# Performance work log

Hardware: AMD Instinct MI355X
Metric: run time of the kernel (lower is better)

Reference implementation:

```python
import jax, jax.numpy as jnp
import numpy as np


def setup_inputs() -> dict:
    key = jax.random.key(0)
    ks = jax.random.split(key, 6)
    B, C, H, W = 16, 192, 224, 224
    MAX_SEG = 196
    img = jax.random.normal(ks[0], (B, 3, H, W), dtype=jnp.float32)
    features = jax.random.normal(ks[1], (B, C, H, W), dtype=jnp.float32)
    segments = jax.random.randint(ks[2], (B, H, W), 0, MAX_SEG, dtype=jnp.int64)
    centroid_coords = jax.random.uniform(ks[3], (B, MAX_SEG, 2), dtype=jnp.float32) * jnp.array([W, H], dtype=jnp.float32)
    pos_W = jax.random.normal(ks[4], (2, C), dtype=jnp.float32) * 0.02
    pos_b = jax.random.normal(ks[5], (C,), dtype=jnp.float32) * 0.02
    return {"img": img, "features": features, "segments": segments,
            "centroid_coords": centroid_coords, "pos_W": pos_W, "pos_b": pos_b,
            "max_segments": MAX_SEG}


def reference(img, features, segments, centroid_coords, pos_W, pos_b, max_segments):
    B, C, Hf, Wf = features.shape
    H, W = img.shape[2], img.shape[3]
    # flatten pixels: [B*Hf*Wf, C]
    feats_flat = features.transpose(0, 2, 3, 1).reshape(-1, C)
    # per-batch-unique segment ids: b * max_segments + seg
    seg_flat = segments.reshape(B, Hf * Wf)
    uniq_ids = (jnp.arange(B, dtype=seg_flat.dtype)[:, None] * max_segments + seg_flat).reshape(-1)
    dim_size = B * max_segments
    # scatter_mean = segment_sum / clamp(count, 1)
    sums = jax.ops.segment_sum(feats_flat, uniq_ids, num_segments=dim_size)
    counts = jax.ops.segment_sum(jnp.ones((feats_flat.shape[0],), feats_flat.dtype),
                                 uniq_ids, num_segments=dim_size)
    embeddings = (sums / jnp.maximum(counts, 1.0)[:, None]).reshape(B, max_segments, C)
    # positional embedding of normalized centroids (x/W, y/H)
    scale = jnp.array([1.0 / W, 1.0 / H], dtype=centroid_coords.dtype)
    pos = (centroid_coords * scale) @ pos_W + pos_b  # [B, n_centroids, C]
    # pad/truncate pos to max_segments (here n_centroids == max_segments)
    n_centroids = pos.shape[1]
    if n_centroids > max_segments:
        pos_padded = pos[:, :max_segments, :]
    else:
        pos_padded = jnp.zeros((B, max_segments, C), pos.dtype).at[:, :n_centroids, :].set(pos)
    return embeddings + pos_padded
```

## Files before the change

### kernel.cpp

```cpp
#include <hip/hip_runtime.h>

#define BATCH 16
#define CHAN 192
#define HW 50176
#define NSEG 196
#define NSEGT 13
#define PIXSPLIT 8
#define PPB (HW / PIXSPLIT)
#define KSTEPS (PPB / 32)

typedef __attribute__((ext_vector_type(8))) short short8;
typedef __attribute__((ext_vector_type(4))) float f32x4;
typedef __attribute__((ext_vector_type(4))) int   i32x4;

__device__ __forceinline__ short bfc(float x) {
    unsigned u = __float_as_uint(x);
    return (short)((u + 0x8000u) >> 16);
}

__global__ __launch_bounds__(384, 3) void accum_mfma(
        const float* __restrict__ feat,
        const int*   __restrict__ seg,
        float*       __restrict__ out) {
    __shared__ short8 abuf[NSEGT * 64];

    const int tid  = threadIdx.x;
    const int wave = tid >> 6;
    const int lane = tid & 63;
    const int quad = lane >> 4;
    const int m    = lane & 15;

    const int b      = blockIdx.z;
    const int cbase  = (blockIdx.y * 6 + wave) * 16;
    const int pstart = blockIdx.x * PPB;

    const int*   sptr = seg  + (size_t)b * HW + pstart;
    const float* fptr = feat + ((size_t)b * CHAN + cbase + m) * HW + pstart;

    f32x4 acc[NSEGT];
#pragma unroll
    for (int t = 0; t < NSEGT; ++t) acc[t] = (f32x4)0.0f;

    i32x4 s0 = *(const i32x4*)(sptr + quad * 8);
    i32x4 s1 = *(const i32x4*)(sptr + quad * 8 + 4);
    f32x4 f0 = *(const f32x4*)(fptr + quad * 8);
    f32x4 f1 = *(const f32x4*)(fptr + quad * 8 + 4);

    for (int kk = 0; kk < KSTEPS; ++kk) {
        __syncthreads();
        const int sv[8] = {s0.x, s0.y, s0.z, s0.w, s1.x, s1.y, s1.z, s1.w};
        for (int t = wave; t < NSEGT; t += 6) {
            const int target = t * 16 + m;
            short8 af;
#pragma unroll
            for (int j = 0; j < 8; ++j)
                af[j] = (sv[j] == target) ? (short)0x3F80 : (short)0;
            abuf[t * 64 + lane] = af;
        }
        __syncthreads();

        short8 bf;
        bf[0] = bfc(f0.x); bf[1] = bfc(f0.y); bf[2] = bfc(f0.z); bf[3] = bfc(f0.w);
        bf[4] = bfc(f1.x); bf[5] = bfc(f1.y); bf[6] = bfc(f1.z); bf[7] = bfc(f1.w);

        const int pn = (kk + 1 < KSTEPS ? kk + 1 : kk) * 32;
        s0 = *(const i32x4*)(sptr + pn + quad * 8);
        s1 = *(const i32x4*)(sptr + pn + quad * 8 + 4);
        f0 = *(const f32x4*)(fptr + pn + quad * 8);
        f1 = *(const f32x4*)(fptr + pn + quad * 8 + 4);

#pragma unroll
        for (int t = 0; t < NSEGT; ++t) {
            short8 af = abuf[t * 64 + lane];
            acc[t] = __builtin_amdgcn_mfma_f32_16x16x32_bf16(af, bf, acc[t], 0, 0, 0);
        }
    }

    float* obase = out + ((size_t)b * NSEG) * CHAN + cbase + m;
#pragma unroll
    for (int t = 0; t < NSEGT; ++t) {
#pragma unroll
        for (int r = 0; r < 4; ++r) {
            const int s = t * 16 + quad * 4 + r;
            if (s < NSEG) atomicAdd(obase + (size_t)s * CHAN, acc[t][r]);
        }
    }
}

__global__ __launch_bounds__(256) void count_kernel(const int* __restrict__ seg,
                                                    int* __restrict__ counts) {
    __shared__ int cnt[NSEG];
    const int tid = threadIdx.x;
    if (tid < NSEG) cnt[tid] = 0;
    __syncthreads();
    const int b = blockIdx.y;
    const int4* sp = (const int4*)(seg + (size_t)b * HW + blockIdx.x * 1024);
    int4 s4 = sp[tid];
    atomicAdd(&cnt[s4.x], 1);
    atomicAdd(&cnt[s4.y], 1);
    atomicAdd(&cnt[s4.z], 1);
    atomicAdd(&cnt[s4.w], 1);
    __syncthreads();
    if (tid < NSEG) atomicAdd(&counts[b * NSEG + tid], cnt[tid]);
}

__global__ __launch_bounds__(256) void finalize_kernel(float* __restrict__ out,
                                                       const int* __restrict__ counts,
                                                       const float* __restrict__ coords,
                                                       const float* __restrict__ posW,
                                                       const float* __restrict__ posb) {
    const int idx = blockIdx.x * 256 + threadIdx.x;
    if (idx >= BATCH * NSEG * CHAN) return;
    const int c = idx % CHAN;
    const int s = (idx / CHAN) % NSEG;
    const int b = idx / (CHAN * NSEG);
    const float cntf = (float)max(counts[b * NSEG + s], 1);
    const float x = coords[(b * NSEG + s) * 2 + 0] * (1.0f / 224.0f);
    const float y = coords[(b * NSEG + s) * 2 + 1] * (1.0f / 224.0f);
    const float pos = x * posW[c] + y * posW[CHAN + c] + posb[c];
    out[idx] = out[idx] / cntf + pos;
}

extern "C" void kernel_launch(void* const* d_in, const int* in_sizes, int n_in,
                              void* d_out, int out_size, void* d_ws, size_t ws_size,
                              hipStream_t stream) {
    const float* feat   = (const float*)d_in[1];
    const int*   seg    = (const int*)d_in[2];
    const float* coords = (const float*)d_in[3];
    const float* posW   = (const float*)d_in[4];
    const float* posb   = (const float*)d_in[5];
    float* out    = (float*)d_out;
    int*   counts = (int*)d_ws;

    hipMemsetAsync(out, 0, (size_t)BATCH * NSEG * CHAN * sizeof(float), stream);
    hipMemsetAsync(counts, 0, (size_t)BATCH * NSEG * sizeof(int), stream);

    count_kernel<<<dim3(HW / 1024, BATCH), 256, 0, stream>>>(seg, counts);
    accum_mfma<<<dim3(PIXSPLIT, 2, BATCH), 384, 0, stream>>>(feat, seg, out);

    const int n = BATCH * NSEG * CHAN;
    finalize_kernel<<<dim3((n + 255) / 256), 256, 0, stream>>>(out, counts, coords, posW, posb);
}
```

Before: 948.5 us.

## Replace one-hot MFMA segment sum with LDS atomic scatter accumulation

Drops the bf16 one-hot-matrix MFMA formulation and instead scatters fp32 features into a padded per-block LDS table of segment sums with shared-memory atomics, then flushes the table to global memory with atomics. The per-segment count is folded into the same kernel, which removes the separate count kernel, and counts become floats. This avoids the 13x redundant one-hot MFMA work and the bf16 rounding. In exchange it relies on LDS atomic throughput under contention and uses about 77KB of LDS per 1024-thread block, which limits occupancy.

```diff
diff --git a/kernel.cpp b/kernel.cpp
--- a/kernel.cpp
+++ b/kernel.cpp
@@ -4,108 +4,75 @@
 #define CHAN 192
 #define HW 50176
 #define NSEG 196
-#define NSEGT 13
-#define PIXSPLIT 8
-#define PPB (HW / PIXSPLIT)
-#define KSTEPS (PPB / 32)
+#define CHALF 96
+#define PAD 97
+#define PIXCHUNK 3136
+#define NGROUP 49
+#define CPW 6
+#define CNT_ROW (NSEG * PAD)
+#define LDS_FLOATS (NSEG * PAD + NSEG)
 
-typedef __attribute__((ext_vector_type(8))) short short8;
-typedef __attribute__((ext_vector_type(4))) float f32x4;
-typedef __attribute__((ext_vector_type(4))) int   i32x4;
-
-__device__ __forceinline__ short bfc(float x) {
-    unsigned u = __float_as_uint(x);
-    return (short)((u + 0x8000u) >> 16);
-}
-
-__global__ __launch_bounds__(384, 3) void accum_mfma(
+__global__ __launch_bounds__(1024, 8) void accum_scatter(
         const float* __restrict__ feat,
         const int*   __restrict__ seg,
-        float*       __restrict__ out) {
-    __shared__ short8 abuf[NSEGT * 64];
+        float*       __restrict__ out,
+        float*       __restrict__ cnt) {
+    __shared__ float lds[LDS_FLOATS];
 
-    const int tid  = threadIdx.x;
-    const int wave = tid >> 6;
-    const int lane = tid & 63;
-    const int quad = lane >> 4;
-    const int m    = lane & 15;
+    const int tid   = threadIdx.x;
+    const int wave  = tid >> 6;
+    const int lane  = tid & 63;
+    const int b     = blockIdx.z;
+    const int cbase = blockIdx.y * CHALF;
+    const int pstart = blockIdx.x * PIXCHUNK;
+    const int lc0   = wave * CPW;
 
-    const int b      = blockIdx.z;
-    const int cbase  = (blockIdx.y * 6 + wave) * 16;
-    const int pstart = blockIdx.x * PPB;
+    for (int i = tid; i < LDS_FLOATS; i += 1024) lds[i] = 0.0f;
+    __syncthreads();
 
-    const int*   sptr = seg  + (size_t)b * HW + pstart;
-    const float* fptr = feat + ((size_t)b * CHAN + cbase + m) * HW + pstart;
+    const int*   sp  = seg  + (size_t)b * HW + pstart + lane;
+    const float* fp0 = feat + ((size_t)b * CHAN + cbase + lc0) * HW + pstart + lane;
+    const bool docount = (blockIdx.y == 0) && (wave == 0);
 
-    f32x4 acc[NSEGT];
+    int   s_cur = sp[0];
+    float v_cur[CPW];
 #pragma unroll
-    for (int t = 0; t < NSEGT; ++t) acc[t] = (f32x4)0.0f;
+    for (int j = 0; j < CPW; ++j) v_cur[j] = fp0[(size_t)j * HW];
 
-    i32x4 s0 = *(const i32x4*)(sptr + quad * 8);
-    i32x4 s1 = *(const i32x4*)(sptr + quad * 8 + 4);
-    f32x4 f0 = *(const f32x4*)(fptr + quad * 8);
-    f32x4 f1 = *(const f32x4*)(fptr + quad * 8 + 4);
+    for (int g = 0; g < NGROUP; ++g) {
+        int   s_nxt = 0;
+        float v_nxt[CPW];
+        if (g + 1 < NGROUP) {
+            const int poff = (g + 1) * 64;
+            s_nxt = sp[poff];
+            const float* fp = fp0 + poff;
+#pragma unroll
+            for (int j = 0; j < CPW; ++j) v_nxt[j] = fp[(size_t)j * HW];
+        }
 
-    for (int kk = 0; kk < KSTEPS; ++kk) {
-        __syncthreads();
-        const int sv[8] = {s0.x, s0.y, s0.z, s0.w, s1.x, s1.y, s1.z, s1.w};
-        for (int t = wave; t < NSEGT; t += 6) {
-            const int target = t * 16 + m;
-            short8 af;
+        if (docount) atomicAdd(lds + CNT_ROW + s_cur, 1.0f);
+        float* lrow = lds + s_cur * PAD + lc0;
 #pragma unroll
-            for (int j = 0; j < 8; ++j)
-                af[j] = (sv[j] == target) ? (short)0x3F80 : (short)0;
-            abuf[t * 64 + lane] = af;
-        }
-        __syncthreads();
+        for (int j = 0; j < CPW; ++j) atomicAdd(lrow + j, v_cur[j]);
 
-        short8 bf;
-        bf[0] = bfc(f0.x); bf[1] = bfc(f0.y); bf[2] = bfc(f0.z); bf[3] = bfc(f0.w);
-        bf[4] = bfc(f1.x); bf[5] = bfc(f1.y); bf[6] = bfc(f1.z); bf[7] = bfc(f1.w);
+        s_cur = s_nxt;
+#pragma unroll
+        for (int j = 0; j < CPW; ++j) v_cur[j] = v_nxt[j];
+    }
+    __syncthreads();
 
-        const int pn = (kk + 1 < KSTEPS ? kk + 1 : kk) * 32;
-        s0 = *(const i32x4*)(sptr + pn + quad * 8);
-        s1 = *(const i32x4*)(sptr + pn + quad * 8 + 4);
-        f0 = *(const f32x4*)(fptr + pn + quad * 8);
-        f1 = *(const f32x4*)(fptr + pn + quad * 8 + 4);
-
-#pragma unroll
-        for (int t = 0; t < NSEGT; ++t) {
-            short8 af = abuf[t * 64 + lane];
-            acc[t] = __builtin_amdgcn_mfma_f32_16x16x32_bf16(af, bf, acc[t], 0, 0, 0);
-        }
+    float* obase = out + ((size_t)b * NSEG) * CHAN + cbase;
+    for (int i = tid; i < NSEG * CHALF; i += 1024) {
+        const int s  = i / CHALF;
+        const int lc = i - s * CHALF;
+        atomicAdd(obase + (size_t)s * CHAN + lc, lds[s * PAD + lc]);
     }
-
-    float* obase = out + ((size_t)b * NSEG) * CHAN + cbase + m;
-#pragma unroll
-    for (int t = 0; t < NSEGT; ++t) {
-#pragma unroll
-        for (int r = 0; r < 4; ++r) {
-            const int s = t * 16 + quad * 4 + r;
-            if (s < NSEG) atomicAdd(obase + (size_t)s * CHAN, acc[t][r]);
-        }
-    }
-}
-
-__global__ __launch_bounds__(256) void count_kernel(const int* __restrict__ seg,
-                                                    int* __restrict__ counts) {
-    __shared__ int cnt[NSEG];
-    const int tid = threadIdx.x;
-    if (tid < NSEG) cnt[tid] = 0;
-    __syncthreads();
-    const int b = blockIdx.y;
-    const int4* sp = (const int4*)(seg + (size_t)b * HW + blockIdx.x * 1024);
-    int4 s4 = sp[tid];
-    atomicAdd(&cnt[s4.x], 1);
-    atomicAdd(&cnt[s4.y], 1);
-    atomicAdd(&cnt[s4.z], 1);
-    atomicAdd(&cnt[s4.w], 1);
-    __syncthreads();
-    if (tid < NSEG) atomicAdd(&counts[b * NSEG + tid], cnt[tid]);
+    if (blockIdx.y == 0 && tid < NSEG)
+        atomicAdd(cnt + b * NSEG + tid, lds[CNT_ROW + tid]);
 }
 
 __global__ __launch_bounds__(256) void finalize_kernel(float* __restrict__ out,
-                                                       const int* __restrict__ counts,
+                                                       const float* __restrict__ counts,
                                                        const float* __restrict__ coords,
                                                        const float* __restrict__ posW,
                                                        const float* __restrict__ posb) {
@@ -114,7 +81,7 @@
     const int c = idx % CHAN;
     const int s = (idx / CHAN) % NSEG;
     const int b = idx / (CHAN * NSEG);
-    const float cntf = (float)max(counts[b * NSEG + s], 1);
+    const float cntf = fmaxf(counts[b * NSEG + s], 1.0f);
     const float x = coords[(b * NSEG + s) * 2 + 0] * (1.0f / 224.0f);
     const float y = coords[(b * NSEG + s) * 2 + 1] * (1.0f / 224.0f);
     const float pos = x * posW[c] + y * posW[CHAN + c] + posb[c];
@@ -130,13 +97,12 @@
     const float* posW   = (const float*)d_in[4];
     const float* posb   = (const float*)d_in[5];
     float* out    = (float*)d_out;
-    int*   counts = (int*)d_ws;
+    float* counts = (float*)d_ws;
 
     hipMemsetAsync(out, 0, (size_t)BATCH * NSEG * CHAN * sizeof(float), stream);
-    hipMemsetAsync(counts, 0, (size_t)BATCH * NSEG * sizeof(int), stream);
+    hipMemsetAsync(counts, 0, (size_t)BATCH * NSEG * sizeof(float), stream);
 
-    count_kernel<<<dim3(HW / 1024, BATCH), 256, 0, stream>>>(seg, counts);
-    accum_mfma<<<dim3(PIXSPLIT, 2, BATCH), 384, 0, stream>>>(feat, seg, out);
+    accum_scatter<<<dim3(16, 2, BATCH), 1024, 0, stream>>>(feat, seg, out, counts);
 
     const int n = BATCH * NSEG * CHAN;
     finalize_kernel<<<dim3((n + 255) / 256), 256, 0, stream>>>(out, counts, coords, posW, posb);
```

Result: slower. 1.403 ms (+47.9%).

## Build one-hot operands in registers, fuse counting, and reduce partials instead of atomics

Applied to the files above, without the earlier changes.

Removes the shared-memory one-hot staging buffer and both block barriers per k-step, so each lane now builds its one-hot A fragments in registers. Segment counting moves into the accumulation kernel, done by one wave per block, which removes a separate launch. The pixel split doubles to give more blocks, and when the workspace is large enough each block writes its partial sums to a buffer that a fused reduce/finalize kernel adds up, replacing the global float atomics. The cost is redundant compare work in every wave, extra partial-buffer traffic, and a serialized count path in wave 0.

```diff
diff --git a/kernel.cpp b/kernel.cpp
--- a/kernel.cpp
+++ b/kernel.cpp
@@ -5,7 +5,7 @@
 #define HW 50176
 #define NSEG 196
 #define NSEGT 13
-#define PIXSPLIT 8
+#define PIXSPLIT 16
 #define PPB (HW / PIXSPLIT)
 #define KSTEPS (PPB / 32)
 
@@ -21,8 +21,10 @@
 __global__ __launch_bounds__(384, 3) void accum_mfma(
         const float* __restrict__ feat,
         const int*   __restrict__ seg,
-        float*       __restrict__ out) {
-    __shared__ short8 abuf[NSEGT * 64];
+        float*       __restrict__ dst,
+        int*         __restrict__ counts,
+        const int partial) {
+    __shared__ int scnt[NSEG];
 
     const int tid  = threadIdx.x;
     const int wave = tid >> 6;
@@ -33,6 +35,11 @@
     const int b      = blockIdx.z;
     const int cbase  = (blockIdx.y * 6 + wave) * 16;
     const int pstart = blockIdx.x * PPB;
+
+    const bool docount = (blockIdx.y == 0) && (wave == 0);
+    if (docount) {
+        for (int i = lane; i < NSEG; i += 64) scnt[i] = 0;
+    }
 
     const int*   sptr = seg  + (size_t)b * HW + pstart;
     const float* fptr = feat + ((size_t)b * CHAN + cbase + m) * HW + pstart;
@@ -47,61 +54,85 @@
     f32x4 f1 = *(const f32x4*)(fptr + quad * 8 + 4);
 
     for (int kk = 0; kk < KSTEPS; ++kk) {
-        __syncthreads();
         const int sv[8] = {s0.x, s0.y, s0.z, s0.w, s1.x, s1.y, s1.z, s1.w};
-        for (int t = wave; t < NSEGT; t += 6) {
-            const int target = t * 16 + m;
-            short8 af;
-#pragma unroll
-            for (int j = 0; j < 8; ++j)
-                af[j] = (sv[j] == target) ? (short)0x3F80 : (short)0;
-            abuf[t * 64 + lane] = af;
-        }
-        __syncthreads();
 
         short8 bf;
         bf[0] = bfc(f0.x); bf[1] = bfc(f0.y); bf[2] = bfc(f0.z); bf[3] = bfc(f0.w);
         bf[4] = bfc(f1.x); bf[5] = bfc(f1.y); bf[6] = bfc(f1.z); bf[7] = bfc(f1.w);
 
+        if (docount && m == 0) {
+#pragma unroll
+            for (int j = 0; j < 8; ++j) atomicAdd(&scnt[sv[j]], 1);
+        }
+
         const int pn = (kk + 1 < KSTEPS ? kk + 1 : kk) * 32;
-        s0 = *(const i32x4*)(sptr + pn + quad * 8);
-        s1 = *(const i32x4*)(sptr + pn + quad * 8 + 4);
-        f0 = *(const f32x4*)(fptr + pn + quad * 8);
-        f1 = *(const f32x4*)(fptr + pn + quad * 8 + 4);
+        i32x4 s0n = *(const i32x4*)(sptr + pn + quad * 8);
+        i32x4 s1n = *(const i32x4*)(sptr + pn + quad * 8 + 4);
+        f32x4 f0n = *(const f32x4*)(fptr + pn + quad * 8);
+        f32x4 f1n = *(const f32x4*)(fptr + pn + quad * 8 + 4);
+
+        int d[8];
+#pragma unroll
+        for (int j = 0; j < 8; ++j) d[j] = sv[j] - m;
 
 #pragma unroll
         for (int t = 0; t < NSEGT; ++t) {
-            short8 af = abuf[t * 64 + lane];
+            short8 af;
+#pragma unroll
+            for (int j = 0; j < 8; ++j)
+                af[j] = (d[j] == t * 16) ? (short)0x3F80 : (short)0;
             acc[t] = __builtin_amdgcn_mfma_f32_16x16x32_bf16(af, bf, acc[t], 0, 0, 0);
         }
+
+        s0 = s0n; s1 = s1n; f0 = f0n; f1 = f1n;
     }
 
-    float* obase = out + ((size_t)b * NSEG) * CHAN + cbase + m;
+    if (partial) {
+        float* obase = dst + (((size_t)blockIdx.x * BATCH + b) * NSEG) * CHAN + cbase + m;
 #pragma unroll
-    for (int t = 0; t < NSEGT; ++t) {
+        for (int t = 0; t < NSEGT; ++t) {
 #pragma unroll
-        for (int r = 0; r < 4; ++r) {
-            const int s = t * 16 + quad * 4 + r;
-            if (s < NSEG) atomicAdd(obase + (size_t)s * CHAN, acc[t][r]);
+            for (int r = 0; r < 4; ++r) {
+                const int s = t * 16 + quad * 4 + r;
+                if (s < NSEG) obase[(size_t)s * CHAN] = acc[t][r];
+            }
         }
+    } else {
+        float* obase = dst + ((size_t)b * NSEG) * CHAN + cbase + m;
+#pragma unroll
+        for (int t = 0; t < NSEGT; ++t) {
+#pragma unroll
+            for (int r = 0; r < 4; ++r) {
+                const int s = t * 16 + quad * 4 + r;
+                if (s < NSEG) atomicAdd(obase + (size_t)s * CHAN, acc[t][r]);
+            }
+        }
+    }
+    if (docount) {
+        for (int i = lane; i < NSEG; i += 64) atomicAdd(&counts[b * NSEG + i], scnt[i]);
     }
 }
 
-__global__ __launch_bounds__(256) void count_kernel(const int* __restrict__ seg,
-                                                    int* __restrict__ counts) {
-    __shared__ int cnt[NSEG];
-    const int tid = threadIdx.x;
-    if (tid < NSEG) cnt[tid] = 0;
-    __syncthreads();
-    const int b = blockIdx.y;
-    const int4* sp = (const int4*)(seg + (size_t)b * HW + blockIdx.x * 1024);
-    int4 s4 = sp[tid];
-    atomicAdd(&cnt[s4.x], 1);
-    atomicAdd(&cnt[s4.y], 1);
-    atomicAdd(&cnt[s4.z], 1);
-    atomicAdd(&cnt[s4.w], 1);
-    __syncthreads();
-    if (tid < NSEG) atomicAdd(&counts[b * NSEG + tid], cnt[tid]);
+__global__ __launch_bounds__(256) void reduce_fin(const float* __restrict__ part,
+                                                  const int* __restrict__ counts,
+                                                  const float* __restrict__ coords,
+                                                  const float* __restrict__ posW,
+                                                  const float* __restrict__ posb,
+                                                  float* __restrict__ out) {
+    const int idx = blockIdx.x * 256 + threadIdx.x;
+    if (idx >= BATCH * NSEG * CHAN) return;
+    const int c = idx % CHAN;
+    const int s = (idx / CHAN) % NSEG;
+    const int b = idx / (CHAN * NSEG);
+    float sum = 0.0f;
+#pragma unroll
+    for (int p = 0; p < PIXSPLIT; ++p)
+        sum += part[(size_t)p * (BATCH * NSEG * CHAN) + idx];
+    const float cntf = (float)max(counts[b * NSEG + s], 1);
+    const float x = coords[(b * NSEG + s) * 2 + 0] * (1.0f / 224.0f);
+    const float y = coords[(b * NSEG + s) * 2 + 1] * (1.0f / 224.0f);
+    const float pos = x * posW[c] + y * posW[CHAN + c] + posb[c];
+    out[idx] = sum / cntf + pos;
 }
 
 __global__ __launch_bounds__(256) void finalize_kernel(float* __restrict__ out,
@@ -132,12 +163,21 @@
     float* out    = (float*)d_out;
     int*   counts = (int*)d_ws;
 
-    hipMemsetAsync(out, 0, (size_t)BATCH * NSEG * CHAN * sizeof(float), stream);
+    const size_t part_off   = 12800;
+    const size_t part_bytes = (size_t)PIXSPLIT * BATCH * NSEG * CHAN * sizeof(float);
+    float* part = (float*)((char*)d_ws + part_off);
+    const bool use_part = ws_size >= part_off + part_bytes;
+
     hipMemsetAsync(counts, 0, (size_t)BATCH * NSEG * sizeof(int), stream);
+    if (!use_part)
+        hipMemsetAsync(out, 0, (size_t)BATCH * NSEG * CHAN * sizeof(float), stream);
 
-    count_kernel<<<dim3(HW / 1024, BATCH), 256, 0, stream>>>(seg, counts);
-    accum_mfma<<<dim3(PIXSPLIT, 2, BATCH), 384, 0, stream>>>(feat, seg, out);
+    accum_mfma<<<dim3(PIXSPLIT, 2, BATCH), 384, 0, stream>>>(
+        feat, seg, use_part ? part : out, counts, use_part ? 1 : 0);
 
     const int n = BATCH * NSEG * CHAN;
-    finalize_kernel<<<dim3((n + 255) / 256), 256, 0, stream>>>(out, counts, coords, posW, posb);
+    if (use_part)
+        reduce_fin<<<dim3((n + 255) / 256), 256, 0, stream>>>(part, counts, coords, posW, posb, out);
+    else
+        finalize_kernel<<<dim3((n + 255) / 256), 256, 0, stream>>>(out, counts, coords, posW, posb);
 }
```

After: 887.5 us. 6.4% less time.
